# Kernel optimization log

Measured on AMD Instinct MI355X. Metric: run time of the kernel, lower is better.

## Reference

```python
import jax, jax.numpy as jnp
import numpy as np

N_NODES = 20000
HIDDEN = 128
MSG = 64
N_EDGES = 320000
TAU = 0.5
EPS = 1e-10


def setup_inputs() -> dict:
    key = jax.random.key(0)
    ks = jax.random.split(key, 12)
    two_msg = 2 * MSG
    return {
        "feat": jax.random.normal(ks[0], (N_NODES, HIDDEN), jnp.float32),
        "h": jax.random.normal(ks[1], (N_NODES, HIDDEN), jnp.float32),
        "src": jax.random.randint(ks[2], (N_EDGES,), 0, N_NODES),
        "dst": jax.random.randint(ks[3], (N_EDGES,), 0, N_NODES),
        "u": jax.random.uniform(ks[4], (N_EDGES, MSG, 2), jnp.float32),
        "W_enc": jax.random.normal(ks[5], (two_msg, 2 * HIDDEN), jnp.float32) * (2 * HIDDEN) ** -0.5,
        "b_enc": jnp.zeros((two_msg,), jnp.float32),
        "W_dec": jax.random.normal(ks[6], (two_msg, two_msg), jnp.float32) * two_msg ** -0.5,
        "b_dec": jnp.zeros((two_msg,), jnp.float32),
        "W_ih": jax.random.normal(ks[7], (3 * HIDDEN, HIDDEN + two_msg), jnp.float32) * (HIDDEN + two_msg) ** -0.5,
        "W_hh": jax.random.normal(ks[8], (3 * HIDDEN, HIDDEN), jnp.float32) * HIDDEN ** -0.5,
        "b_ih": jnp.zeros((3 * HIDDEN,), jnp.float32),
        "b_hh": jnp.zeros((3 * HIDDEN,), jnp.float32),
    }


def reference(feat, h, src, dst, u, W_enc, b_enc, W_dec, b_dec, W_ih, W_hh, b_ih, b_hh):
    N, H = h.shape
    two_msg = W_enc.shape[0]
    msg = two_msg // 2

    # --- per-edge message encoding (hidden state detached, as in original) ---
    h_det = jax.lax.stop_gradient(h)
    e_in = jnp.concatenate([feat[src], h_det[src]], axis=1)          # [E, 2H]
    logits = (e_in @ W_enc.T + b_enc).reshape(-1, msg, 2)            # [E, msg, 2]

    # gumbel-softmax, tau=0.5, hard=True (straight-through)
    g = -jnp.log(-jnp.log(u + EPS) + EPS)
    y = jax.nn.softmax((logits + g) / TAU, axis=-1)
    onehot = jax.nn.one_hot(jnp.argmax(y, axis=-1), 2, dtype=y.dtype)
    m = (y + jax.lax.stop_gradient(onehot - y)).reshape(-1, two_msg)  # [E, 2*msg]

    # --- segment-max aggregation (elementwise OR since msgs are 0/1) ---
    seg = jax.ops.segment_max(m, dst, num_segments=N)                 # [N, 2*msg]
    deg = jax.ops.segment_sum(jnp.ones_like(dst), dst, num_segments=N)
    c = jnp.where((deg > 0)[:, None], seg, 0.0)                       # zero for isolated nodes

    # --- GRUCell update: input = [feat, f_dec(c)] ---
    x = jnp.concatenate([feat, c @ W_dec.T + b_dec], axis=1)          # [N, H + 2*msg]
    gi = x @ W_ih.T + b_ih
    gh = h @ W_hh.T + b_hh
    ir, iz, inn = jnp.split(gi, 3, axis=1)
    hr, hz, hn = jnp.split(gh, 3, axis=1)
    r = jax.nn.sigmoid(ir + hr)
    z = jax.nn.sigmoid(iz + hz)
    n = jnp.tanh(inn + r * hn)
    h_new = (1.0 - z) * n + z * h
    return (h_new, h_new)
```

## Files before the change

### kernel.cpp

```cpp
#include <hip/hip_runtime.h>
#include <stdint.h>

#define NN   20000
#define NNP  20096
#define NE   320000
#define GEPS 1e-10f

typedef __attribute__((ext_vector_type(8))) __bf16 bf16x8;
typedef __attribute__((ext_vector_type(4))) float f32x4;

__device__ __forceinline__ float fsigmoid(float x) { return 1.f / (1.f + __expf(-x)); }
__device__ __forceinline__ float ftanh(float x)    { return 1.f - 2.f / (__expf(2.f * x) + 1.f); }


__global__ __launch_bounds__(256) void prep_k(
    const float* __restrict__ feat,  const float* __restrict__ hst,
    const float* __restrict__ W_enc, const float* __restrict__ b_enc,
    const float* __restrict__ W_dec, const float* __restrict__ b_dec,
    const float* __restrict__ W_ih,  const float* __restrict__ W_hh,
    const float* __restrict__ b_ih,  const float* __restrict__ b_hh,
    __bf16* __restrict__ B1h, __bf16* __restrict__ B1l,
    __bf16* __restrict__ B2h, __bf16* __restrict__ B2l,
    float* __restrict__ bias1, float* __restrict__ bias2,
    float* __restrict__ W_comb, ulonglong2* __restrict__ mask2,
    __bf16* __restrict__ Aph, __bf16* __restrict__ Apl)
{
    const int b = blockIdx.x, t = threadIdx.x;
    if (b < 128) {
        const int src = (b >> 6) * 64 + (b & 31) * 2 + ((b >> 5) & 1);
        const float v = W_enc[src * 256 + t];
        const __bf16 hi = (__bf16)v;
        const int kt = t >> 5, fkh = (t >> 3) & 3, e = t & 7;
        const size_t idx = ((size_t)(kt * 4 + fkh) * 128 + b) * 8 + e;
        B1h[idx] = hi;
        B1l[idx] = (__bf16)(v - (float)hi);
    } else if (b < 640) {
        const int r2 = b - 128;
        const int nb = r2 >> 7, rem = r2 & 127, g = rem >> 5, jj = rem & 31;
        const int j = nb * 32 + jj;
        const int k = t;
        float v;
        if (g == 0)      v = (k < 128) ? W_ih[j * 256 + k]         : W_hh[j * 128 + (k - 128)];
        else if (g == 1) v = (k < 128) ? W_ih[(128 + j) * 256 + k] : W_hh[(128 + j) * 128 + (k - 128)];
        else if (g == 2) v = (k < 128) ? W_ih[(256 + j) * 256 + k] : 0.f;
        else             v = (k < 128) ? 0.f                       : W_hh[(256 + j) * 128 + (k - 128)];
        const __bf16 hi = (__bf16)v;
        const int kt = t >> 5, fkh = (t >> 3) & 3, e = t & 7;
        const size_t idx = ((size_t)(kt * 4 + fkh) * 512 + r2) * 8 + e;
        B2h[idx] = hi;
        B2l[idx] = (__bf16)(v - (float)hi);
    } else if (b < 832) {
        const int idx = (b - 640) * 256 + t;
        const int o = idx >> 7, k = idx & 127;
        float s = 0.f;
        for (int l = 0; l < 128; ++l)
            s += W_ih[o * 256 + 128 + l] * W_dec[l * 128 + k];
        W_comb[idx] = s;
    } else if (b < 835) {
        __shared__ float bd[128];
        if (t < 128) {
            float s = b_dec[t];
            for (int k = 0; k < 128; ++k) s += W_dec[t * 128 + k];
            bd[t] = s;
        }
        __syncthreads();
        const int g = (b - 832) * 256 + t;
        if (g < 128) {
            bias1[g] = b_enc[(g >> 6) * 64 + (g & 31) * 2 + ((g >> 5) & 1)];
        } else if (g < 640) {
            const int c2 = g - 128;
            const int nb = c2 >> 7, rem = c2 & 127, gg = rem >> 5, jj = rem & 31;
            const int j = nb * 32 + jj;
            float v;
            if (gg == 3) v = b_hh[256 + j];
            else {
                const int o = gg * 128 + j;
                float s = (gg == 2) ? b_ih[o] : (b_ih[o] + b_hh[o]);
                for (int l = 0; l < 128; ++l) s += W_ih[o * 256 + 128 + l] * bd[l];
                v = s;
            }
            bias2[c2] = v;
        }
    } else if (b < 914) {
        const int i = (b - 835) * 256 + t;
        if (i < NN) mask2[i] = make_ulonglong2(0ull, 0ull);
    } else {
        const int blk = b - 914;
        const int row = blk * 8 + (t & 7);
        const int k0  = (t >> 3) * 8;
        float x[8];
        if (row < NN) {
            const float* sp = (k0 < 128) ? (feat + (size_t)row * 128 + k0)
                                         : (hst  + (size_t)row * 128 + (k0 - 128));
            const float4 v0 = *(const float4*)sp;
            const float4 v1 = *(const float4*)(sp + 4);
            x[0] = v0.x; x[1] = v0.y; x[2] = v0.z; x[3] = v0.w;
            x[4] = v1.x; x[5] = v1.y; x[6] = v1.z; x[7] = v1.w;
        } else {
#pragma unroll
            for (int i = 0; i < 8; ++i) x[i] = 0.f;
        }
        bf16x8 hi, lo;
#pragma unroll
        for (int i = 0; i < 8; ++i) {
            const __bf16 hv = (__bf16)x[i];
            hi[i] = hv;
            lo[i] = (__bf16)(x[i] - (float)hv);
        }
        const int kt = k0 >> 5, fkh = (k0 >> 3) & 3;
        const size_t idx = ((size_t)(kt * 4 + fkh) * NNP + row) * 8;
        *(bf16x8*)(Aph + idx) = hi;
        *(bf16x8*)(Apl + idx) = lo;
    }
}

__global__ __launch_bounds__(256) void gemm_rtab(
    const __bf16* __restrict__ Aph, const __bf16* __restrict__ Apl,
    const __bf16* __restrict__ B1h, const __bf16* __restrict__ B1l,
    const float* __restrict__ bias1, float* __restrict__ rtab)
{
    const int t = threadIdx.x, lane = t & 63, wid = t >> 6;
    const int m0 = blockIdx.x * 32;
    const int wm = (wid & 1) * 16;
    const int cgn = wid >> 1;
    const int wn = cgn * 64;
    const int fr = lane & 15, fkh = lane >> 4;

    f32x4 acc[4];
#pragma unroll
    for (int j = 0; j < 4; ++j) acc[j] = (f32x4){0.f, 0.f, 0.f, 0.f};

    for (int kt = 0; kt < 8; ++kt) {
        const size_t ab = (size_t)(kt * 4 + fkh) * NNP;
        const size_t bb = (size_t)(kt * 4 + fkh) * 128;
        const size_t ro = (ab + m0 + wm + fr) * 8;
        const bf16x8 ah = *(const bf16x8*)(Aph + ro);
        const bf16x8 al = *(const bf16x8*)(Apl + ro);
#pragma unroll
        for (int nf = 0; nf < 4; ++nf) {
            const size_t rb = (bb + wn + nf * 16 + fr) * 8;
            const bf16x8 bh = *(const bf16x8*)(B1h + rb);
            const bf16x8 bl = *(const bf16x8*)(B1l + rb);
            acc[nf] = __builtin_amdgcn_mfma_f32_16x16x32_bf16(ah, bh, acc[nf], 0, 0, 0);
            acc[nf] = __builtin_amdgcn_mfma_f32_16x16x32_bf16(al, bh, acc[nf], 0, 0, 0);
            acc[nf] = __builtin_amdgcn_mfma_f32_16x16x32_bf16(ah, bl, acc[nf], 0, 0, 0);
        }
    }

#pragma unroll
    for (int nf = 0; nf < 2; ++nf) {
        const int c0 = wn + nf * 16 + fr;
        const float b0 = bias1[c0], b1 = bias1[c0 + 32];
        const int j = cgn * 32 + nf * 16 + fr;
#pragma unroll
        for (int rr = 0; rr < 4; ++rr) {
            const int gr = m0 + wm + (lane >> 4) * 4 + rr;
            if (gr < NN)
                rtab[(size_t)gr * 64 + j] =
                    __expf((acc[nf + 2][rr] + b1) - (acc[nf][rr] + b0));
        }
    }
}

#define EPW 16
__global__ __launch_bounds__(256) void edge_k(
    const float* __restrict__ u, const int* __restrict__ src,
    const int* __restrict__ dst, const float* __restrict__ rtab,
    unsigned long long* __restrict__ masks)
{
    const int wv = __builtin_amdgcn_readfirstlane(blockIdx.x * 4 + (threadIdx.x >> 6));
    const int lane = threadIdx.x & 63;
    const int e0 = wv * EPW;

    float2 uu[EPW];
    float  rr[EPW];
    int    dd[EPW];
#pragma unroll
    for (int i = 0; i < EPW; ++i) {
        const int e = e0 + i;
        uu[i] = *(const float2*)(u + (size_t)e * 128 + lane * 2);
        rr[i] = rtab[(size_t)src[e] * 64 + lane];
        dd[i] = dst[e];
    }
#pragma unroll
    for (int i = 0; i < EPW; ++i) {
        const float a0 = GEPS - __logf(uu[i].x + GEPS);
        const float a1 = GEPS - __logf(uu[i].y + GEPS);
        const unsigned long long mone = __ballot(rr[i] * a0 > a1);
        if (lane == 0) {
            atomicOr(&masks[(size_t)dd[i] * 2 + 1], mone);
            atomicOr(&masks[(size_t)dd[i] * 2 + 0], ~mone);
        }
    }
}

__global__ __launch_bounds__(256) void gemm_gates(
    const __bf16* __restrict__ Aph, const __bf16* __restrict__ Apl,
    const __bf16* __restrict__ B2h,
    const float* __restrict__ bias2, const unsigned long long* __restrict__ masks,
    const float* __restrict__ W_comb, const float* __restrict__ h,
    float* __restrict__ out)
{
    const int bid = blockIdx.x;
    const int nb = bid & 3;
    const int m0 = (bid >> 2) * 64;

    const int t = threadIdx.x, lane = t & 63, wid = t >> 6;
    const int wm = (wid & 1) * 32;
    const int jh = wid >> 1;
    const int fr = lane & 15, fkh = lane >> 4;

    f32x4 acc[2][4];
#pragma unroll
    for (int i = 0; i < 2; ++i)
#pragma unroll
        for (int j = 0; j < 4; ++j) acc[i][j] = (f32x4){0.f, 0.f, 0.f, 0.f};

    for (int kt = 0; kt < 8; ++kt) {
        const size_t ab = (size_t)(kt * 4 + fkh) * NNP;
        const size_t bb = (size_t)(kt * 4 + fkh) * 512;
        bf16x8 ah[2], al[2];
#pragma unroll
        for (int mf = 0; mf < 2; ++mf) {
            const size_t ro = (ab + m0 + wm + mf * 16 + fr) * 8;
            ah[mf] = *(const bf16x8*)(Aph + ro);
            al[mf] = *(const bf16x8*)(Apl + ro);
        }
#pragma unroll
        for (int g = 0; g < 4; ++g) {
            const size_t ro = (bb + nb * 128 + g * 32 + jh * 16 + fr) * 8;
            const bf16x8 bh = *(const bf16x8*)(B2h + ro);
#pragma unroll
            for (int mf = 0; mf < 2; ++mf) {
                acc[mf][g] = __builtin_amdgcn_mfma_f32_16x16x32_bf16(ah[mf], bh, acc[mf][g], 0, 0, 0);
                acc[mf][g] = __builtin_amdgcn_mfma_f32_16x16x32_bf16(al[mf], bh, acc[mf][g], 0, 0, 0);
            }
        }
    }

    float bia[4];
#pragma unroll
    for (int g = 0; g < 4; ++g) bia[g] = bias2[nb * 128 + g * 32 + jh * 16 + fr];
    const int j = nb * 32 + jh * 16 + fr;

#pragma unroll
    for (int mf = 0; mf < 2; ++mf)
#pragma unroll
        for (int rr = 0; rr < 4; ++rr) {
            const int gr = m0 + wm + mf * 16 + (lane >> 4) * 4 + rr;
            if (gr >= NN) continue;
            const unsigned long long ze = ~masks[(size_t)gr * 2 + 0];
            const unsigned long long zo = ~masks[(size_t)gr * 2 + 1];
            float rp = acc[mf][0][rr] + bia[0];
            float zp = acc[mf][1][rr] + bia[1];
            float ip = acc[mf][2][rr] + bia[2];
            float hp = acc[mf][3][rr] + bia[3];
            if (ze | zo) {
                unsigned long long bz = ze;
#pragma unroll 1
                while (bz) {
                    const int k = __builtin_ctzll(bz); bz &= bz - 1;
                    const int bit = 2 * k;
                    rp -= W_comb[(size_t)j * 128 + bit];
                    zp -= W_comb[(size_t)(128 + j) * 128 + bit];
                    ip -= W_comb[(size_t)(256 + j) * 128 + bit];
                }
                bz = zo;
#pragma unroll 1
                while (bz) {
                    const int k = __builtin_ctzll(bz); bz &= bz - 1;
                    const int bit = 2 * k + 1;
                    rp -= W_comb[(size_t)j * 128 + bit];
                    zp -= W_comb[(size_t)(128 + j) * 128 + bit];
                    ip -= W_comb[(size_t)(256 + j) * 128 + bit];
                }
            }
            const float hv = h[(size_t)gr * 128 + j];
            const float rg = fsigmoid(rp);
            const float zg = fsigmoid(zp);
            const float nv = ftanh(ip + rg * hp);
            const float o = (1.f - zg) * nv + zg * hv;
            out[(size_t)gr * 128 + j] = o;
            out[(size_t)(NN + gr) * 128 + j] = o;
        }
}

extern "C" void kernel_launch(void* const* d_in, const int* in_sizes, int n_in,
                              void* d_out, int out_size, void* d_ws, size_t ws_size,
                              hipStream_t stream) {
    const float* feat  = (const float*)d_in[0];
    const float* h     = (const float*)d_in[1];
    const int*   src   = (const int*)d_in[2];
    const int*   dst   = (const int*)d_in[3];
    const float* u     = (const float*)d_in[4];
    const float* W_enc = (const float*)d_in[5];
    const float* b_enc = (const float*)d_in[6];
    const float* W_dec = (const float*)d_in[7];
    const float* b_dec = (const float*)d_in[8];
    const float* W_ih  = (const float*)d_in[9];
    const float* W_hh  = (const float*)d_in[10];
    const float* b_ih  = (const float*)d_in[11];
    const float* b_hh  = (const float*)d_in[12];
    float* out = (float*)d_out;
    (void)in_sizes; (void)n_in; (void)out_size; (void)ws_size;

    char* ws = (char*)d_ws;
    float*              rtab   = (float*)(ws + 0);
    unsigned long long* masks  = (unsigned long long*)(ws + 5120000);
    __bf16*             B1h    = (__bf16*)(ws + 5440000);
    __bf16*             B1l    = (__bf16*)(ws + 5505536);
    __bf16*             B2h    = (__bf16*)(ws + 5571072);
    __bf16*             B2l    = (__bf16*)(ws + 5833216);
    float*              bias1  = (float*)(ws + 6095360);
    float*              bias2  = (float*)(ws + 6095872);
    float*              W_comb = (float*)(ws + 6097920);
    __bf16*             Aph    = (__bf16*)(ws + 6294528);
    __bf16*             Apl    = (__bf16*)(ws + 16583680);

    prep_k<<<914 + NNP / 8, 256, 0, stream>>>(
        feat, h, W_enc, b_enc, W_dec, b_dec, W_ih, W_hh, b_ih, b_hh,
        B1h, B1l, B2h, B2l, bias1, bias2, W_comb, (ulonglong2*)masks, Aph, Apl);

    gemm_rtab<<<NNP / 32, 256, 0, stream>>>(Aph, Apl, B1h, B1l, bias1, rtab);

    edge_k<<<NE / (4 * EPW), 256, 0, stream>>>(u, src, dst, rtab, masks);

    gemm_gates<<<(NNP / 64) * 4, 256, 0, stream>>>(Aph, Apl, B2h, bias2, masks, W_comb, h, out);
}
```

Measured before the change: 92.68 us.

## Fuse activation bf16 split conversion into the rtab GEMM and drop unused B2l

The feat/h hi/lo bf16 split is now computed inside gemm_rtab straight from fp32 inputs rather than in prep_k. gemm_rtab still writes the packed Aph/Apl buffers for the later gates GEMM. Each block now covers 64 rows with every wave computing all 128 output columns, which avoids a separate pass that writes and then rereads the split activations. The unused B2l low-part weights are no longer produced, and the workspace is repacked to match.

```diff
diff --git a/kernel.cpp b/kernel.cpp
--- a/kernel.cpp
+++ b/kernel.cpp
@@ -14,16 +14,14 @@
 
 
 __global__ __launch_bounds__(256) void prep_k(
-    const float* __restrict__ feat,  const float* __restrict__ hst,
     const float* __restrict__ W_enc, const float* __restrict__ b_enc,
     const float* __restrict__ W_dec, const float* __restrict__ b_dec,
     const float* __restrict__ W_ih,  const float* __restrict__ W_hh,
     const float* __restrict__ b_ih,  const float* __restrict__ b_hh,
     __bf16* __restrict__ B1h, __bf16* __restrict__ B1l,
-    __bf16* __restrict__ B2h, __bf16* __restrict__ B2l,
+    __bf16* __restrict__ B2h,
     float* __restrict__ bias1, float* __restrict__ bias2,
-    float* __restrict__ W_comb, ulonglong2* __restrict__ mask2,
-    __bf16* __restrict__ Aph, __bf16* __restrict__ Apl)
+    float* __restrict__ W_comb, ulonglong2* __restrict__ mask2)
 {
     const int b = blockIdx.x, t = threadIdx.x;
     if (b < 128) {
@@ -44,11 +42,9 @@
         else if (g == 1) v = (k < 128) ? W_ih[(128 + j) * 256 + k] : W_hh[(128 + j) * 128 + (k - 128)];
         else if (g == 2) v = (k < 128) ? W_ih[(256 + j) * 256 + k] : 0.f;
         else             v = (k < 128) ? 0.f                       : W_hh[(256 + j) * 128 + (k - 128)];
-        const __bf16 hi = (__bf16)v;
         const int kt = t >> 5, fkh = (t >> 3) & 3, e = t & 7;
         const size_t idx = ((size_t)(kt * 4 + fkh) * 512 + r2) * 8 + e;
-        B2h[idx] = hi;
-        B2l[idx] = (__bf16)(v - (float)hi);
+        B2h[idx] = (__bf16)v;
     } else if (b < 832) {
         const int idx = (b - 640) * 256 + t;
         const int o = idx >> 7, k = idx & 127;
@@ -81,17 +77,34 @@
             }
             bias2[c2] = v;
         }
-    } else if (b < 914) {
+    } else {
         const int i = (b - 835) * 256 + t;
         if (i < NN) mask2[i] = make_ulonglong2(0ull, 0ull);
-    } else {
-        const int blk = b - 914;
-        const int row = blk * 8 + (t & 7);
-        const int k0  = (t >> 3) * 8;
+    }
+}
+
+__global__ __launch_bounds__(256) void gemm_rtab(
+    const float* __restrict__ feat, const float* __restrict__ hst,
+    const __bf16* __restrict__ B1h, const __bf16* __restrict__ B1l,
+    const float* __restrict__ bias1, float* __restrict__ rtab,
+    __bf16* __restrict__ Aph, __bf16* __restrict__ Apl)
+{
+    const int t = threadIdx.x, lane = t & 63, wid = t >> 6;
+    const int m0 = blockIdx.x * 64;
+    const int wm = wid * 16;
+    const int fr = lane & 15, fkh = lane >> 4;
+    const int row = m0 + wm + fr;
+
+    f32x4 acc[8];
+#pragma unroll
+    for (int j = 0; j < 8; ++j) acc[j] = (f32x4){0.f, 0.f, 0.f, 0.f};
+
+    for (int kt = 0; kt < 8; ++kt) {
+        const int kc = kt * 32 + fkh * 8;
         float x[8];
         if (row < NN) {
-            const float* sp = (k0 < 128) ? (feat + (size_t)row * 128 + k0)
-                                         : (hst  + (size_t)row * 128 + (k0 - 128));
+            const float* sp = (kc < 128) ? (feat + (size_t)row * 128 + kc)
+                                         : (hst  + (size_t)row * 128 + (kc - 128));
             const float4 v0 = *(const float4*)sp;
             const float4 v1 = *(const float4*)(sp + 4);
             x[0] = v0.x; x[1] = v0.y; x[2] = v0.z; x[3] = v0.w;
@@ -100,45 +113,21 @@
 #pragma unroll
             for (int i = 0; i < 8; ++i) x[i] = 0.f;
         }
-        bf16x8 hi, lo;
+        bf16x8 ah, al;
 #pragma unroll
         for (int i = 0; i < 8; ++i) {
             const __bf16 hv = (__bf16)x[i];
-            hi[i] = hv;
-            lo[i] = (__bf16)(x[i] - (float)hv);
-        }
-        const int kt = k0 >> 5, fkh = (k0 >> 3) & 3;
-        const size_t idx = ((size_t)(kt * 4 + fkh) * NNP + row) * 8;
-        *(bf16x8*)(Aph + idx) = hi;
-        *(bf16x8*)(Apl + idx) = lo;
-    }
-}
-
-__global__ __launch_bounds__(256) void gemm_rtab(
-    const __bf16* __restrict__ Aph, const __bf16* __restrict__ Apl,
-    const __bf16* __restrict__ B1h, const __bf16* __restrict__ B1l,
-    const float* __restrict__ bias1, float* __restrict__ rtab)
-{
-    const int t = threadIdx.x, lane = t & 63, wid = t >> 6;
-    const int m0 = blockIdx.x * 32;
-    const int wm = (wid & 1) * 16;
-    const int cgn = wid >> 1;
-    const int wn = cgn * 64;
-    const int fr = lane & 15, fkh = lane >> 4;
-
-    f32x4 acc[4];
-#pragma unroll
-    for (int j = 0; j < 4; ++j) acc[j] = (f32x4){0.f, 0.f, 0.f, 0.f};
-
-    for (int kt = 0; kt < 8; ++kt) {
-        const size_t ab = (size_t)(kt * 4 + fkh) * NNP;
+            ah[i] = hv;
+            al[i] = (__bf16)(x[i] - (float)hv);
+        }
+        const size_t aidx = ((size_t)(kt * 4 + fkh) * NNP + row) * 8;
+        *(bf16x8*)(Aph + aidx) = ah;
+        *(bf16x8*)(Apl + aidx) = al;
+
         const size_t bb = (size_t)(kt * 4 + fkh) * 128;
-        const size_t ro = (ab + m0 + wm + fr) * 8;
-        const bf16x8 ah = *(const bf16x8*)(Aph + ro);
-        const bf16x8 al = *(const bf16x8*)(Apl + ro);
-#pragma unroll
-        for (int nf = 0; nf < 4; ++nf) {
-            const size_t rb = (bb + wn + nf * 16 + fr) * 8;
+#pragma unroll
+        for (int nf = 0; nf < 8; ++nf) {
+            const size_t rb = (bb + nf * 16 + fr) * 8;
             const bf16x8 bh = *(const bf16x8*)(B1h + rb);
             const bf16x8 bl = *(const bf16x8*)(B1l + rb);
             acc[nf] = __builtin_amdgcn_mfma_f32_16x16x32_bf16(ah, bh, acc[nf], 0, 0, 0);
@@ -148,13 +137,14 @@
     }
 
 #pragma unroll
-    for (int nf = 0; nf < 2; ++nf) {
-        const int c0 = wn + nf * 16 + fr;
+    for (int np = 0; np < 4; ++np) {
+        const int nf = (np >> 1) * 4 + (np & 1);
+        const int c0 = nf * 16 + fr;
         const float b0 = bias1[c0], b1 = bias1[c0 + 32];
-        const int j = cgn * 32 + nf * 16 + fr;
+        const int j = (nf >> 2) * 32 + (nf & 1) * 16 + fr;
 #pragma unroll
         for (int rr = 0; rr < 4; ++rr) {
-            const int gr = m0 + wm + (lane >> 4) * 4 + rr;
+            const int gr = m0 + wm + fkh * 4 + rr;
             if (gr < NN)
                 rtab[(size_t)gr * 64 + j] =
                     __expf((acc[nf + 2][rr] + b1) - (acc[nf][rr] + b0));
@@ -310,18 +300,17 @@
     __bf16*             B1h    = (__bf16*)(ws + 5440000);
     __bf16*             B1l    = (__bf16*)(ws + 5505536);
     __bf16*             B2h    = (__bf16*)(ws + 5571072);
-    __bf16*             B2l    = (__bf16*)(ws + 5833216);
-    float*              bias1  = (float*)(ws + 6095360);
-    float*              bias2  = (float*)(ws + 6095872);
-    float*              W_comb = (float*)(ws + 6097920);
-    __bf16*             Aph    = (__bf16*)(ws + 6294528);
-    __bf16*             Apl    = (__bf16*)(ws + 16583680);
-
-    prep_k<<<914 + NNP / 8, 256, 0, stream>>>(
-        feat, h, W_enc, b_enc, W_dec, b_dec, W_ih, W_hh, b_ih, b_hh,
-        B1h, B1l, B2h, B2l, bias1, bias2, W_comb, (ulonglong2*)masks, Aph, Apl);
-
-    gemm_rtab<<<NNP / 32, 256, 0, stream>>>(Aph, Apl, B1h, B1l, bias1, rtab);
+    float*              bias1  = (float*)(ws + 5833216);
+    float*              bias2  = (float*)(ws + 5833728);
+    float*              W_comb = (float*)(ws + 5835776);
+    __bf16*             Aph    = (__bf16*)(ws + 6032384);
+    __bf16*             Apl    = (__bf16*)(ws + 16321536);
+
+    prep_k<<<835 + (NN + 255) / 256, 256, 0, stream>>>(
+        W_enc, b_enc, W_dec, b_dec, W_ih, W_hh, b_ih, b_hh,
+        B1h, B1l, B2h, bias1, bias2, W_comb, (ulonglong2*)masks);
+
+    gemm_rtab<<<NNP / 64, 256, 0, stream>>>(feat, h, B1h, B1l, bias1, rtab, Aph, Apl);
 
     edge_k<<<NE / (4 * EPW), 256, 0, stream>>>(u, src, dst, rtab, masks);
 
```

After: 104.4 us. 1.13x slower.
